# Kernel optimization log

Measured on AMD Instinct MI355X. Metric: run time of the kernel, lower is better.

## Reference

```python
import jax, jax.numpy as jnp
import numpy as np

B, WIN, DM, DG, K = 32, 128, 1024, 64, 15  # batch, win_size(node feat dim), d_model(#nodes), graph embed, top_k


def setup_inputs() -> dict:
    key = jax.random.key(0)
    ks = jax.random.split(key, 7)
    sc_in = 1.0 / np.sqrt(WIN)
    return {
        "x": jax.random.normal(ks[0], (B, WIN, DM), jnp.float32),
        "Wq": jax.random.normal(ks[1], (DG, WIN), jnp.float32) * sc_in,
        "bq": jax.random.normal(ks[2], (DG,), jnp.float32) * 0.02,
        "Wk": jax.random.normal(ks[3], (DG, WIN), jnp.float32) * sc_in,
        "bk": jax.random.normal(ks[4], (DG,), jnp.float32) * 0.02,
        "Wg": jax.random.normal(ks[5], (WIN, WIN), jnp.float32) * sc_in,  # GCNConv lin weight [out,in]
        "bg": jax.random.normal(ks[6], (WIN,), jnp.float32) * 0.02,
    }


def _gcn_one(nf, Wq, bq, Wk, bk, Wg, bg):
    # nf: [N, F] node features (N = d_model, F = win_size)
    N = nf.shape[0]
    q = nf @ Wq.T + bq                      # [N, DG]
    k = nf @ Wk.T + bk                      # [N, DG]
    scores = (q @ k.T) * (1.0 / np.sqrt(DG))  # [N, N]
    scores = jnp.where(jnp.eye(N, dtype=bool), -jnp.inf, scores)
    _, tgt = jax.lax.top_k(scores, K)       # [N, K] top-k neighbors per source node
    src = jnp.repeat(jnp.arange(N), K)      # [N*K]
    tgt = tgt.reshape(-1)                   # [N*K]
    loops = jnp.arange(N)
    # manual self loops (module) + self loops added internally by GCNConv (default add_self_loops=True)
    src_all = jnp.concatenate([src, loops, loops])
    tgt_all = jnp.concatenate([tgt, loops, loops])
    # gcn_norm: degree over target (col) with unit edge weights
    deg = jax.ops.segment_sum(jnp.ones_like(tgt_all, jnp.float32), tgt_all, num_segments=N)
    dinv = jnp.where(deg > 0, jax.lax.rsqrt(deg), 0.0)
    norm = dinv[src_all] * dinv[tgt_all]    # [E]
    h = nf @ Wg.T                           # [N, F] linear transform (no bias inside lin)
    msg = h[src_all] * norm[:, None]        # gather + scale
    out = jax.ops.segment_sum(msg, tgt_all, num_segments=N) + bg  # scatter-add + bias
    return out                              # [N, F]


def reference(x, Wq, bq, Wk, bk, Wg, bg):
    # x: [B, win_size, d_model] -> nodes: [B, d_model, win_size]
    nodes = x.transpose(0, 2, 1)
    h = jax.vmap(lambda nf: _gcn_one(nf, Wq, bq, Wk, bk, Wg, bg))(nodes)  # [B, N, F]
    # n_layers == 1: no ReLU/dropout applied after last layer
    return h.transpose(0, 2, 1)  # [B, win_size, d_model]
```

## Files before the change

### kernel.cpp

```cpp
#include <hip/hip_runtime.h>

#define NBATCH 32
#define NN     1024
#define NF     128
#define NDG    64
#define TOPK   15

#define OFF_QH    ((size_t)0)
#define OFF_QL    ((size_t)4194304)
#define OFF_KH    ((size_t)8388608)
#define OFF_KL    ((size_t)12582912)
#define OFF_H     ((size_t)16777216)
#define OFF_DEG   ((size_t)33554432)
#define OFF_BMP   ((size_t)33685504)
#define OFF_WL    ((size_t)37879808)
#define OFF_TOPK  ((size_t)38010880)
#define OFF_KT32  ((size_t)40239104)
#define OFF_TMP   ((size_t)0)

typedef short s8v  __attribute__((ext_vector_type(8)));
typedef float f4v  __attribute__((ext_vector_type(4)));
typedef unsigned short us8v __attribute__((ext_vector_type(8)));

__device__ inline unsigned short bf16_rne(float f) {
    unsigned u = __float_as_uint(f);
    return (unsigned short)((u + 0x7FFFu + ((u >> 16) & 1u)) >> 16);
}
__device__ inline float bf16_tof(unsigned short h) { return __uint_as_float(((unsigned)h) << 16); }

__device__ inline unsigned pack22(float s) {
    unsigned u   = __float_as_uint(s);
    int      mag = (int)(u & 0x7FFFFFFFu);
    int      t   = mag - 0x38800000;
    t = t < 0 ? 0 : (t > 0x07FFFFFF ? 0x07FFFFFF : t);
    unsigned ts = (unsigned)t >> 6;
    return ((int)u < 0) ? (0x1FFFFFu - ts) : (0x200000u | ts);
}
__device__ inline float dec22(unsigned val22) {
    bool pos = (val22 & 0x200000u) != 0;
    unsigned ts = pos ? (val22 & 0x1FFFFFu) : (0x1FFFFFu - (val22 & 0x1FFFFFu));
    float f = __uint_as_float((ts << 6) + 0x38800000u);
    return pos ? f : -f;
}

__global__ __launch_bounds__(256) void k_prep(
    const float* __restrict__ x, const float* __restrict__ bq, const float* __restrict__ bk,
    const float* __restrict__ Wq, const float* __restrict__ Wk,
    const float* __restrict__ Wg,
    unsigned short* __restrict__ qh, unsigned short* __restrict__ ql,
    unsigned short* __restrict__ kh, unsigned short* __restrict__ kl,
    float* __restrict__ kT32,
    float* __restrict__ h,
    uint4* __restrict__ zbase, int zn)
{
    __shared__ float xs[64 * 129];
    const int t = threadIdx.x;
    const int l = t & 63;
    const int w = t >> 6;
    const int uw = __builtin_amdgcn_readfirstlane(w);
    const int bid = blockIdx.x;
    const int lid = (bid & 7) * 128 + (bid >> 3);
    const int b    = lid >> 5;
    const int half = (lid >> 4) & 1;
    const int n0   = (lid & 15) * 64;

    {
        int lid0 = bid * 256 + t;
        for (int i = lid0; i < zn; i += 262144)
            zbase[i] = make_uint4(0u, 0u, 0u, 0u);
    }

    {
        const int j = t & 63, fg = t >> 6;
        for (int ff = 0; ff < 32; ++ff) {
            int f = fg + ff * 4;
            xs[j * 129 + f] = x[((size_t)b * NF + f) * NN + n0 + j];
        }
    }
    __syncthreads();

    {
        const int d0 = half * 32 + uw * 8;
        float accq[8], acck[8];
        #pragma unroll
        for (int dd = 0; dd < 8; ++dd) {
            accq[dd] = bq[d0 + dd];
            acck[dd] = bk[d0 + dd];
        }
        for (int fc = 0; fc < 32; ++fc) {
            float x0 = xs[l * 129 + fc * 4 + 0];
            float x1 = xs[l * 129 + fc * 4 + 1];
            float x2 = xs[l * 129 + fc * 4 + 2];
            float x3 = xs[l * 129 + fc * 4 + 3];
            #pragma unroll
            for (int dd = 0; dd < 8; ++dd) {
                int d = d0 + dd;
                const float* wq = &Wq[d * NF + fc * 4];
                const float* wk = &Wk[d * NF + fc * 4];
                accq[dd] += x0 * wq[0] + x1 * wq[1] + x2 * wq[2] + x3 * wq[3];
                acck[dd] += x0 * wk[0] + x1 * wk[1] + x2 * wk[2] + x3 * wk[3];
            }
        }
        #pragma unroll
        for (int dd = 0; dd < 8; ++dd)
            kT32[((size_t)b * NDG + d0 + dd) * NN + n0 + l] = acck[dd];
        us8v qh0, ql0, kh0, kl0;
        #pragma unroll
        for (int dd = 0; dd < 8; ++dd) {
            unsigned short h1 = bf16_rne(accq[dd]);
            unsigned short l1 = bf16_rne(accq[dd] - bf16_tof(h1));
            unsigned short h2 = bf16_rne(acck[dd]);
            unsigned short l2 = bf16_rne(acck[dd] - bf16_tof(h2));
            qh0[dd] = h1; ql0[dd] = l1; kh0[dd] = h2; kl0[dd] = l2;
        }
        size_t nb = ((size_t)b * NN + n0 + l) * NDG + d0;
        *(us8v*)&qh[nb] = qh0;
        *(us8v*)&ql[nb] = ql0;
        *(us8v*)&kh[nb] = kh0;
        *(us8v*)&kl[nb] = kl0;
    }

    {
        const int fp0 = half * 64 + uw * 16;
        float acc[16];
        #pragma unroll
        for (int i = 0; i < 16; ++i) acc[i] = 0.f;
        for (int fc = 0; fc < 32; ++fc) {
            float x0 = xs[l * 129 + fc * 4 + 0];
            float x1 = xs[l * 129 + fc * 4 + 1];
            float x2 = xs[l * 129 + fc * 4 + 2];
            float x3 = xs[l * 129 + fc * 4 + 3];
            #pragma unroll
            for (int ff = 0; ff < 16; ++ff) {
                const float* wg = &Wg[(fp0 + ff) * NF + fc * 4];
                acc[ff] += x0 * wg[0] + x1 * wg[1] + x2 * wg[2] + x3 * wg[3];
            }
        }
        __syncthreads();
        #pragma unroll
        for (int ff = 0; ff < 16; ++ff) xs[l * 129 + fp0 + ff] = acc[ff];
        __syncthreads();
        for (int r = 0; r < 16; ++r) {
            int idx = t + 256 * r;
            int n = idx >> 6, f = idx & 63;
            h[((size_t)b * NN + n0 + n) * NF + half * 64 + f] = xs[n * 129 + half * 64 + f];
        }
    }
}

__device__ inline void bsort64_2(unsigned& va, unsigned& vb, int l) {
    #pragma unroll
    for (int k = 2; k <= 64; k <<= 1) {
        #pragma unroll
        for (int j = k >> 1; j >= 1; j >>= 1) {
            unsigned pa = (unsigned)__shfl_xor((int)va, j, 64);
            unsigned pb = (unsigned)__shfl_xor((int)vb, j, 64);
            bool tm = ((l & k) == 0) == ((l & j) == 0);
            unsigned ha = va > pa ? va : pa, la = va > pa ? pa : va;
            unsigned hb = vb > pb ? vb : pb, lb = vb > pb ? pb : vb;
            va = tm ? ha : la;
            vb = tm ? hb : lb;
        }
    }
}

__global__ __launch_bounds__(256) void k_score(
    const unsigned short* __restrict__ qh, const unsigned short* __restrict__ ql,
    const unsigned short* __restrict__ kh, const unsigned short* __restrict__ kl,
    const float* __restrict__ bk,
    unsigned int* __restrict__ bmp,
    int* __restrict__ topk, int* __restrict__ wl_cnt, int* __restrict__ wl)
{
    __shared__ unsigned slots[64 * 96];
    __shared__ int      cntw[64 * 4];
    const int t = threadIdx.x, l = t & 63, w = t >> 6;
    const int bid = blockIdx.x;
    const int lid = (bid & 7) * 64 + (bid >> 3);
    const int b = lid >> 4, row0 = (lid & 15) * 64;
    const int m = l & 15, q4 = l >> 4;

    s8v ah0[4], ah1[4], al0[4], al1[4];
    #pragma unroll
    for (int g = 0; g < 4; ++g) {
        size_t abase = ((size_t)b * NN + row0 + g * 16 + m) * NDG + q4 * 8;
        ah0[g] = *(const s8v*)&qh[abase];
        ah1[g] = *(const s8v*)&qh[abase + 32];
        al0[g] = *(const s8v*)&ql[abase];
        al1[g] = *(const s8v*)&ql[abase + 32];
    }

    float Tr[4][4];
    #pragma unroll
    for (int g = 0; g < 4; ++g) {
        float ssq = 0.f, smn = 0.f;
        #pragma unroll
        for (int j = 0; j < 8; ++j) {
            float q0 = bf16_tof(((us8v)ah0[g])[j]) + bf16_tof(((us8v)al0[g])[j]);
            float q1 = bf16_tof(((us8v)ah1[g])[j]) + bf16_tof(((us8v)al1[g])[j]);
            float b0 = bk[q4 * 8 + j];
            float b1 = bk[q4 * 8 + 32 + j];
            ssq += q0 * q0 + q1 * q1;
            smn += q0 * b0 + q1 * b1;
        }
        ssq += __shfl_xor(ssq, 16, 64); ssq += __shfl_xor(ssq, 32, 64);
        smn += __shfl_xor(smn, 16, 64); smn += __shfl_xor(smn, 32, 64);
        float t8 = smn + 1.8f * __builtin_sqrtf(ssq);
        #pragma unroll
        for (int r = 0; r < 4; ++r)
            Tr[g][r] = __shfl(t8, 4 * q4 + r, 64);
    }

    const int colbase = w * 256;
    int basec[4][4] = {{0,0,0,0},{0,0,0,0},{0,0,0,0},{0,0,0,0}};

    #pragma unroll
    for (int tt = 0; tt < 16; ++tt) {
        const int col = colbase + tt * 16 + m;
        size_t bb = ((size_t)b * NN + col) * NDG + q4 * 8;
        s8v Bh0 = *(const s8v*)&kh[bb];
        s8v Bh1 = *(const s8v*)&kh[bb + 32];
        s8v Bl0 = *(const s8v*)&kl[bb];
        s8v Bl1 = *(const s8v*)&kl[bb + 32];
        #pragma unroll
        for (int g = 0; g < 4; ++g) {
            f4v acc = {0.f, 0.f, 0.f, 0.f};
            acc = __builtin_amdgcn_mfma_f32_16x16x32_bf16(al0[g], Bl0, acc, 0, 0, 0);
            acc = __builtin_amdgcn_mfma_f32_16x16x32_bf16(al1[g], Bl1, acc, 0, 0, 0);
            acc = __builtin_amdgcn_mfma_f32_16x16x32_bf16(ah0[g], Bl0, acc, 0, 0, 0);
            acc = __builtin_amdgcn_mfma_f32_16x16x32_bf16(ah1[g], Bl1, acc, 0, 0, 0);
            acc = __builtin_amdgcn_mfma_f32_16x16x32_bf16(al0[g], Bh0, acc, 0, 0, 0);
            acc = __builtin_amdgcn_mfma_f32_16x16x32_bf16(al1[g], Bh1, acc, 0, 0, 0);
            acc = __builtin_amdgcn_mfma_f32_16x16x32_bf16(ah0[g], Bh0, acc, 0, 0, 0);
            acc = __builtin_amdgcn_mfma_f32_16x16x32_bf16(ah1[g], Bh1, acc, 0, 0, 0);
            #pragma unroll
            for (int r = 0; r < 4; ++r) {
                const int rloc = g * 16 + q4 * 4 + r;
                const int grow = row0 + rloc;
                bool p = (acc[r] >= Tr[g][r]) && (col != grow);
                unsigned long long mk = __ballot(p);
                unsigned w16 = (unsigned)(mk >> (q4 * 16)) & 0xFFFFu;
                int idx = basec[g][r] + __popc(w16 & ((1u << m) - 1u));
                if (p && idx < 24) {
                    float s = acc[r] * 0.125f;
                    slots[rloc * 96 + w * 24 + idx] = (pack22(s) << 10) | (unsigned)(1023 - col);
                }
                basec[g][r] += __popc(w16);
            }
        }
    }
    if (m == 0) {
        #pragma unroll
        for (int g = 0; g < 4; ++g)
            #pragma unroll
            for (int r = 0; r < 4; ++r)
                cntw[(g * 16 + q4 * 4 + r) * 4 + w] = basec[g][r];
    }
    __syncthreads();

    #pragma unroll
    for (int pp = 0; pp < 8; ++pp) {
        const int rA = w * 16 + 2 * pp, rB = rA + 1;
        int a0 = cntw[rA * 4 + 0], a1 = cntw[rA * 4 + 1], a2 = cntw[rA * 4 + 2], a3 = cntw[rA * 4 + 3];
        int b0 = cntw[rB * 4 + 0], b1 = cntw[rB * 4 + 1], b2 = cntw[rB * 4 + 2], b3 = cntw[rB * 4 + 3];
        bool ovA = (a0 > 24) || (a1 > 24) || (a2 > 24) || (a3 > 24);
        bool ovB = (b0 > 24) || (b1 > 24) || (b2 > 24) || (b3 > 24);
        int rawA = a0 + a1 + a2 + a3, rawB = b0 + b1 + b2 + b3;
        a0 = a0 > 24 ? 24 : a0; a1 = a1 > 24 ? 24 : a1; a2 = a2 > 24 ? 24 : a2; a3 = a3 > 24 ? 24 : a3;
        b0 = b0 > 24 ? 24 : b0; b1 = b1 > 24 ? 24 : b1; b2 = b2 > 24 ? 24 : b2; b3 = b3 > 24 ? 24 : b3;
        int PA1 = a0, PA2 = a0 + a1, PA3 = a0 + a1 + a2, CA = PA3 + a3;
        int PB1 = b0, PB2 = b0 + b1, PB3 = b0 + b1 + b2, CB = PB3 + b3;
        bool fbA = ovA || rawA < 16 || rawA > 64;
        bool fbB = ovB || rawB < 16 || rawB > 64;

        int jA = (l >= PA1) + (l >= PA2) + (l >= PA3);
        int jB = (l >= PB1) + (l >= PB2) + (l >= PB3);
        int baseA = jA == 0 ? 0 : (jA == 1 ? PA1 : (jA == 2 ? PA2 : PA3));
        int baseB = jB == 0 ? 0 : (jB == 1 ? PB1 : (jB == 2 ? PB2 : PB3));
        unsigned cva = (l < CA) ? slots[rA * 96 + jA * 24 + (l - baseA)] : 0u;
        unsigned cvb = (l < CB) ? slots[rB * 96 + jB * 24 + (l - baseB)] : 0u;
        bsort64_2(cva, cvb, l);

        #pragma unroll
        for (int rr = 0; rr < 2; ++rr) {
            const int grow = row0 + (rr == 0 ? rA : rB);
            unsigned res   = rr == 0 ? cva : cvb;
            const bool fb  = rr == 0 ? fbA : fbB;

            unsigned r14 = (unsigned)__shfl((int)res, 14, 64);
            unsigned r15 = (unsigned)__shfl((int)res, 15, 64);
            bool flagged;
            if (fb) {
                flagged = true;
            } else {
                float s15 = dec22(r14 >> 10), s16 = dec22(r15 >> 10);
                unsigned e15 = (__float_as_uint(fabsf(s15)) >> 23) & 255u;
                unsigned e16 = (__float_as_uint(fabsf(s16)) >> 23) & 255u;
                unsigned e = e15 > e16 ? e15 : e16;
                float qq = __uint_as_float((e - 17) << 23);
                flagged = (s15 - s16) < (4.f * qq + 1e-4f);
            }
            if (l < 15) {
                int col = fb ? ((grow + 1 + l) & 1023)
                             : (1023 - (int)(res & 1023u));
                atomicOr(&bmp[((size_t)b * NN + col) * 32 + (grow >> 5)], 1u << (grow & 31));
                if (flagged) topk[(b * NN + grow) * 16 + l] = col;
            }
            if (l == 0 && flagged) {
                int idx = atomicAdd(wl_cnt, 1);
                if (idx < 32767) wl[idx] = b * NN + grow;
            }
        }
    }
}

__global__ __launch_bounds__(256) void k_repair(
    const float* __restrict__ x, const float* __restrict__ bq, const float* __restrict__ Wq,
    const float* __restrict__ kT32,
    const int* __restrict__ topk, const int* __restrict__ wl_cnt, const int* __restrict__ wl,
    unsigned int* __restrict__ bmp)
{
    const int t = threadIdx.x, l = t & 63, w = t >> 6;
    __shared__ float  xrow[128];
    __shared__ double qld[64];
    __shared__ double cmax[4];
    __shared__ int    cidx[4];
    __shared__ int    oldset[15], newset[15];
    const double NEGINF = -__builtin_inf();
    int n = wl_cnt[0]; if (n > 32767) n = 32767;

    for (int i = blockIdx.x; i < n; i += 1024) {
        int rg = wl[i];
        int b = rg >> 10, row = rg & 1023;

        __syncthreads();
        if (t < 128) xrow[t] = x[((size_t)b * NF + t) * NN + row];
        if (t < 15) oldset[t] = topk[(b * NN + row) * 16 + t];
        __syncthreads();
        if (t < 64) {
            double acc = (double)bq[t];
            const float* wq = &Wq[t * NF];
            for (int f = 0; f < 128; ++f)
                acc += (double)xrow[f] * (double)wq[f];
            qld[t] = acc;
        }
        __syncthreads();

        const float* kb = &kT32[(size_t)b * NDG * NN];
        const int base = l + 256 * w;
        const int c0 = base, c1 = base + 64, c2 = base + 128, c3 = base + 192;
        double s0 = 0.0, s1 = 0.0, s2 = 0.0, s3 = 0.0;
        float b0 = kb[c0], b1 = kb[c1], b2 = kb[c2], b3 = kb[c3];
        for (int d = 0; d < 64; ++d) {
            float n0, n1, n2, n3;
            if (d < 63) {
                const float* kr = kb + (size_t)(d + 1) * NN;
                n0 = kr[c0]; n1 = kr[c1]; n2 = kr[c2]; n3 = kr[c3];
            }
            double qd = qld[d];
            s0 += qd * (double)b0; s1 += qd * (double)b1;
            s2 += qd * (double)b2; s3 += qd * (double)b3;
            if (d < 63) { b0 = n0; b1 = n1; b2 = n2; b3 = n3; }
        }
        if (c0 == row) s0 = NEGINF;
        if (c1 == row) s1 = NEGINF;
        if (c2 == row) s2 = NEGINF;
        if (c3 == row) s3 = NEGINF;

        for (int it = 0; it < 15; ++it) {
            double lv = NEGINF; int lc = 0x7fffffff;
            if (s0 > lv) { lv = s0; lc = c0; }
            if (s1 > lv) { lv = s1; lc = c1; }
            if (s2 > lv) { lv = s2; lc = c2; }
            if (s3 > lv) { lv = s3; lc = c3; }
            #pragma unroll
            for (int off = 1; off < 64; off <<= 1) {
                double ov = __shfl_xor(lv, off, 64);
                int    oc = __shfl_xor(lc, off, 64);
                if (ov > lv || (ov == lv && oc < lc)) { lv = ov; lc = oc; }
            }
            if (l == 0) { cmax[w] = lv; cidx[w] = lc; }
            __syncthreads();
            if (t == 0) {
                double bv = cmax[0]; int bc = cidx[0];
                #pragma unroll
                for (int ww = 1; ww < 4; ++ww)
                    if (cmax[ww] > bv || (cmax[ww] == bv && cidx[ww] < bc)) { bv = cmax[ww]; bc = cidx[ww]; }
                newset[it] = bc;
            }
            __syncthreads();
            int bc = newset[it];
            if (c0 == bc) s0 = NEGINF;
            if (c1 == bc) s1 = NEGINF;
            if (c2 == bc) s2 = NEGINF;
            if (c3 == bc) s3 = NEGINF;
        }

        if (t < 15) {
            int cn = newset[t];
            bool found = false;
            #pragma unroll
            for (int j = 0; j < 15; ++j) found = found || (oldset[j] == cn);
            if (!found)
                atomicOr(&bmp[((size_t)b * NN + cn) * 32 + (row >> 5)], 1u << (row & 31));
            int co = oldset[t];
            found = false;
            #pragma unroll
            for (int j = 0; j < 15; ++j) found = found || (newset[j] == co);
            if (!found)
                atomicAnd(&bmp[((size_t)b * NN + co) * 32 + (row >> 5)], ~(1u << (row & 31)));
        }
    }
}

__global__ __launch_bounds__(256) void k_deg(const unsigned int* __restrict__ bmp,
                                             int* __restrict__ deg)
{
    int i = blockIdx.x * 256 + threadIdx.x;
    const uint4* p = (const uint4*)(bmp + (size_t)i * 32);
    int s = 0;
    #pragma unroll
    for (int j = 0; j < 8; ++j) {
        uint4 v = p[j];
        s += __popc(v.x) + __popc(v.y) + __popc(v.z) + __popc(v.w);
    }
    deg[i] = s;
}

__global__ __launch_bounds__(128) void k_gather(
    const float* __restrict__ h, const float* __restrict__ bg,
    const int* __restrict__ deg, const unsigned int* __restrict__ bmp,
    float* __restrict__ tmp)
{
    __shared__ int list[1024];
    __shared__ float nrm[1024];
    __shared__ int scnt;
    const int bid = blockIdx.x;
    const int lid = (bid & 7) * 4096 + (bid >> 3);
    const int b = lid >> 10, tgt = lid & 1023;
    const int t = threadIdx.x;
    if (t < 32) {
        unsigned word = bmp[((size_t)b * NN + tgt) * 32 + t];
        int pc = __popc(word);
        int pre = pc;
        #pragma unroll
        for (int d = 1; d < 32; d <<= 1) {
            int o = __shfl_up(pre, d, 32);
            if (t >= d) pre += o;
        }
        if (t == 31) scnt = pre;
        int idx = pre - pc;
        while (word) {
            int s = __ffs(word) - 1;
            word &= word - 1;
            list[idx++] = t * 32 + s;
        }
    }
    __syncthreads();
    const int cnt = scnt;
    for (int e = t; e < cnt; e += 128)
        nrm[e] = rsqrtf((float)(deg[b * NN + list[e]] + 2));
    __syncthreads();
    const int f = t;
    float dt = rsqrtf((float)(deg[b * NN + tgt] + 2));
    float a0 = 0.f, a1 = 0.f, a2 = 0.f, a3 = 0.f;
    int e = 0;
    for (; e + 4 <= cnt; e += 4) {
        a0 += h[((size_t)b * NN + list[e + 0]) * NF + f] * nrm[e + 0];
        a1 += h[((size_t)b * NN + list[e + 1]) * NF + f] * nrm[e + 1];
        a2 += h[((size_t)b * NN + list[e + 2]) * NF + f] * nrm[e + 2];
        a3 += h[((size_t)b * NN + list[e + 3]) * NF + f] * nrm[e + 3];
    }
    for (; e < cnt; ++e)
        a0 += h[((size_t)b * NN + list[e]) * NF + f] * nrm[e];
    float acc = 2.0f * dt * h[((size_t)b * NN + tgt) * NF + f] + ((a0 + a1) + (a2 + a3));
    tmp[((size_t)b * NN + tgt) * NF + f] = bg[f] + dt * acc;
}

__global__ __launch_bounds__(256) void k_transpose(const float* __restrict__ tmp,
                                                   float* __restrict__ out)
{
    __shared__ float tile[32][33];
    const int t = threadIdx.x;
    const int n0 = blockIdx.x * 32, f0 = blockIdx.y * 32, b = blockIdx.z;
    const int c = t & 31, rb = t >> 5;
    #pragma unroll
    for (int i = 0; i < 4; ++i) {
        int r = rb + i * 8;
        tile[r][c] = tmp[((size_t)b * NN + n0 + r) * NF + f0 + c];
    }
    __syncthreads();
    #pragma unroll
    for (int i = 0; i < 4; ++i) {
        int r = rb + i * 8;
        out[((size_t)b * NF + f0 + r) * NN + n0 + c] = tile[c][r];
    }
}

extern "C" void kernel_launch(void* const* d_in, const int* in_sizes, int n_in,
                              void* d_out, int out_size, void* d_ws, size_t ws_size,
                              hipStream_t stream)
{
    const float* x  = (const float*)d_in[0];
    const float* Wq = (const float*)d_in[1];
    const float* bq = (const float*)d_in[2];
    const float* Wk = (const float*)d_in[3];
    const float* bk = (const float*)d_in[4];
    const float* Wg = (const float*)d_in[5];
    const float* bg = (const float*)d_in[6];
    float* out = (float*)d_out;
    char* ws = (char*)d_ws;

    unsigned short* qh = (unsigned short*)(ws + OFF_QH);
    unsigned short* ql = (unsigned short*)(ws + OFF_QL);
    unsigned short* kh = (unsigned short*)(ws + OFF_KH);
    unsigned short* kl = (unsigned short*)(ws + OFF_KL);
    float*          h   = (float*)(ws + OFF_H);
    int*            deg = (int*)(ws + OFF_DEG);
    unsigned int*   bmp = (unsigned int*)(ws + OFF_BMP);
    int*            wlc = (int*)(ws + OFF_WL);
    int*            wl  = wlc + 1;
    int*            tpk = (int*)(ws + OFF_TOPK);
    float*          kT32 = (float*)(ws + OFF_KT32);
    float*          tmp  = (float*)(ws + OFF_TMP);

    k_prep<<<1024, 256, 0, stream>>>(x, bq, bk, Wq, Wk, Wg,
                                     qh, ql, kh, kl, kT32, h,
                                     (uint4*)(ws + OFF_DEG), 270337);
    k_score<<<512, 256, 0, stream>>>(qh, ql, kh, kl, bk, bmp, tpk, wlc, wl);
    k_repair<<<1024, 256, 0, stream>>>(x, bq, Wq, kT32, tpk, wlc, wl, bmp);
    k_deg<<<128, 256, 0, stream>>>(bmp, deg);
    k_gather<<<32768, 128, 0, stream>>>(h, bg, deg, bmp, tmp);
    k_transpose<<<dim3(32, 4, 32), 256, 0, stream>>>(tmp, out);
}
```

Baseline: 259.4 us.

## Fuse gather with output transpose and process 32 targets per block

The gather kernel now handles 32 target nodes per 256-thread block, one wavefront per 8 targets. Each lane computes two features through float2 loads, and source indices and norms are broadcast by wave shuffles instead of shared-memory staging and block barriers. Results are staged in LDS and written straight to the transposed output layout, which removes the separate transpose kernel and the round trip through the temporary buffer. In exchange, per-wave serial work is higher and the grid drops to 1024 blocks, which may reduce latency hiding for the irregular gathers.

```diff
diff --git a/kernel.cpp b/kernel.cpp
--- a/kernel.cpp
+++ b/kernel.cpp
@@ -16,7 +16,6 @@
 #define OFF_WL    ((size_t)37879808)
 #define OFF_TOPK  ((size_t)38010880)
 #define OFF_KT32  ((size_t)40239104)
-#define OFF_TMP   ((size_t)0)
 
 typedef short s8v  __attribute__((ext_vector_type(8)));
 typedef float f4v  __attribute__((ext_vector_type(4)));
@@ -426,73 +425,82 @@
     deg[i] = s;
 }
 
-__global__ __launch_bounds__(128) void k_gather(
+__global__ __launch_bounds__(256) void k_gather(
     const float* __restrict__ h, const float* __restrict__ bg,
     const int* __restrict__ deg, const unsigned int* __restrict__ bmp,
-    float* __restrict__ tmp)
+    float* __restrict__ out)
 {
-    __shared__ int list[1024];
-    __shared__ float nrm[1024];
-    __shared__ int scnt;
+    __shared__ float accs[32 * 130];
+    __shared__ int   lst[4][1024];
+    const int t = threadIdx.x, l = t & 63, w = t >> 6;
     const int bid = blockIdx.x;
-    const int lid = (bid & 7) * 4096 + (bid >> 3);
-    const int b = lid >> 10, tgt = lid & 1023;
-    const int t = threadIdx.x;
-    if (t < 32) {
-        unsigned word = bmp[((size_t)b * NN + tgt) * 32 + t];
+    const int lid = (bid & 7) * 128 + (bid >> 3);
+    const int b = lid >> 5, n0 = (lid & 31) * 32;
+    const float2* __restrict__ h2 = (const float2*)h;
+    const float2 bgv = ((const float2*)bg)[l];
+
+    for (int tg = 0; tg < 8; ++tg) {
+        const int tgt = n0 + w * 8 + tg;
+        unsigned word = (l < 32) ? bmp[((size_t)b * NN + tgt) * 32 + l] : 0u;
         int pc = __popc(word);
         int pre = pc;
         #pragma unroll
         for (int d = 1; d < 32; d <<= 1) {
-            int o = __shfl_up(pre, d, 32);
-            if (t >= d) pre += o;
-        }
-        if (t == 31) scnt = pre;
-        int idx = pre - pc;
-        while (word) {
-            int s = __ffs(word) - 1;
-            word &= word - 1;
-            list[idx++] = t * 32 + s;
-        }
+            int o = __shfl_up(pre, d, 64);
+            if (l >= d) pre += o;
+        }
+        const int cnt = __shfl(pre, 31, 64);
+        if (l < 32) {
+            int idx = pre - pc;
+            while (word) {
+                int s = __ffs(word) - 1;
+                word &= word - 1;
+                lst[w][idx++] = l * 32 + s;
+            }
+        }
+
+        const float dt = rsqrtf((float)(deg[b * NN + tgt] + 2));
+        float2 hs = h2[((size_t)b * NN + tgt) * 64 + l];
+        float a0x = 2.0f * dt * hs.x, a0y = 2.0f * dt * hs.y;
+        float a1x = 0.f, a1y = 0.f, a2x = 0.f, a2y = 0.f, a3x = 0.f, a3y = 0.f;
+
+        for (int base = 0; base < cnt; base += 64) {
+            const int len = (cnt - base) < 64 ? (cnt - base) : 64;
+            int   srcv = (l < len) ? lst[w][base + l] : 0;
+            float nrmv = (l < len) ? rsqrtf((float)(deg[b * NN + srcv] + 2)) : 0.f;
+            int e = 0;
+            for (; e + 4 <= len; e += 4) {
+                int   s0 = __shfl(srcv, e + 0, 64), s1 = __shfl(srcv, e + 1, 64);
+                int   s2 = __shfl(srcv, e + 2, 64), s3 = __shfl(srcv, e + 3, 64);
+                float r0 = __shfl(nrmv, e + 0, 64), r1 = __shfl(nrmv, e + 1, 64);
+                float r2 = __shfl(nrmv, e + 2, 64), r3 = __shfl(nrmv, e + 3, 64);
+                float2 v0 = h2[((size_t)b * NN + s0) * 64 + l];
+                float2 v1 = h2[((size_t)b * NN + s1) * 64 + l];
+                float2 v2 = h2[((size_t)b * NN + s2) * 64 + l];
+                float2 v3 = h2[((size_t)b * NN + s3) * 64 + l];
+                a0x += v0.x * r0; a0y += v0.y * r0;
+                a1x += v1.x * r1; a1y += v1.y * r1;
+                a2x += v2.x * r2; a2y += v2.y * r2;
+                a3x += v3.x * r3; a3y += v3.y * r3;
+            }
+            for (; e < len; ++e) {
+                int   s0 = __shfl(srcv, e, 64);
+                float r0 = __shfl(nrmv, e, 64);
+                float2 v0 = h2[((size_t)b * NN + s0) * 64 + l];
+                a0x += v0.x * r0; a0y += v0.y * r0;
+            }
+        }
+        float rx = bgv.x + dt * (((a0x + a1x) + (a2x + a3x)));
+        float ry = bgv.y + dt * (((a0y + a1y) + (a2y + a3y)));
+        ((float2*)&accs[(w * 8 + tg) * 130])[l] = make_float2(rx, ry);
     }
     __syncthreads();
-    const int cnt = scnt;
-    for (int e = t; e < cnt; e += 128)
-        nrm[e] = rsqrtf((float)(deg[b * NN + list[e]] + 2));
-    __syncthreads();
-    const int f = t;
-    float dt = rsqrtf((float)(deg[b * NN + tgt] + 2));
-    float a0 = 0.f, a1 = 0.f, a2 = 0.f, a3 = 0.f;
-    int e = 0;
-    for (; e + 4 <= cnt; e += 4) {
-        a0 += h[((size_t)b * NN + list[e + 0]) * NF + f] * nrm[e + 0];
-        a1 += h[((size_t)b * NN + list[e + 1]) * NF + f] * nrm[e + 1];
-        a2 += h[((size_t)b * NN + list[e + 2]) * NF + f] * nrm[e + 2];
-        a3 += h[((size_t)b * NN + list[e + 3]) * NF + f] * nrm[e + 3];
-    }
-    for (; e < cnt; ++e)
-        a0 += h[((size_t)b * NN + list[e]) * NF + f] * nrm[e];
-    float acc = 2.0f * dt * h[((size_t)b * NN + tgt) * NF + f] + ((a0 + a1) + (a2 + a3));
-    tmp[((size_t)b * NN + tgt) * NF + f] = bg[f] + dt * acc;
-}
-
-__global__ __launch_bounds__(256) void k_transpose(const float* __restrict__ tmp,
-                                                   float* __restrict__ out)
-{
-    __shared__ float tile[32][33];
-    const int t = threadIdx.x;
-    const int n0 = blockIdx.x * 32, f0 = blockIdx.y * 32, b = blockIdx.z;
-    const int c = t & 31, rb = t >> 5;
-    #pragma unroll
-    for (int i = 0; i < 4; ++i) {
-        int r = rb + i * 8;
-        tile[r][c] = tmp[((size_t)b * NN + n0 + r) * NF + f0 + c];
-    }
-    __syncthreads();
-    #pragma unroll
-    for (int i = 0; i < 4; ++i) {
-        int r = rb + i * 8;
-        out[((size_t)b * NF + f0 + r) * NN + n0 + c] = tile[c][r];
+
+    const int c = t & 31, fg = t >> 5;
+    #pragma unroll
+    for (int i = 0; i < 16; ++i) {
+        int f = fg + i * 8;
+        out[((size_t)b * NF + f) * NN + n0 + c] = accs[c * 130 + f];
     }
 }
 
@@ -521,7 +529,6 @@
     int*            wl  = wlc + 1;
     int*            tpk = (int*)(ws + OFF_TOPK);
     float*          kT32 = (float*)(ws + OFF_KT32);
-    float*          tmp  = (float*)(ws + OFF_TMP);
 
     k_prep<<<1024, 256, 0, stream>>>(x, bq, bk, Wq, Wk, Wg,
                                      qh, ql, kh, kl, kT32, h,
@@ -529,6 +536,5 @@
     k_score<<<512, 256, 0, stream>>>(qh, ql, kh, kl, bk, bmp, tpk, wlc, wl);
     k_repair<<<1024, 256, 0, stream>>>(x, bq, Wq, kT32, tpk, wlc, wl, bmp);
     k_deg<<<128, 256, 0, stream>>>(bmp, deg);
-    k_gather<<<32768, 128, 0, stream>>>(h, bg, deg, bmp, tmp);
-    k_transpose<<<dim3(32, 4, 32), 256, 0, stream>>>(tmp, out);
-}
+    k_gather<<<1024, 256, 0, stream>>>(h, bg, deg, bmp, out);
+}
```

Result: no change. 263.9 us (+1.8%).
